# Kernel optimization log

Hardware: AMD Instinct MI355X
Metric: run time of the kernel (lower is better)

## Reference

```python
import jax, jax.numpy as jnp
import numpy as np

H = 1024   # hidden_dim
D = 256    # output_dim
T = 64     # output_len
B = 256    # batch
FC1, FC2 = 1024, 512
EPS = 1e-5


def setup_inputs() -> dict:
    key = jax.random.key(0)
    ks = iter(jax.random.split(key, 32))
    s = 0.05
    p = {}
    p['hidden'] = jax.random.normal(next(ks), (2, B, H), jnp.float32)
    # GRU layer 0: input D -> hidden H ; layer 1: H -> H
    p['W_ih0'] = jax.random.normal(next(ks), (3 * H, D), jnp.float32) * s
    p['W_hh0'] = jax.random.normal(next(ks), (3 * H, H), jnp.float32) * s
    p['b_ih0'] = jax.random.normal(next(ks), (3 * H,), jnp.float32) * s
    p['b_hh0'] = jax.random.normal(next(ks), (3 * H,), jnp.float32) * s
    p['W_ih1'] = jax.random.normal(next(ks), (3 * H, H), jnp.float32) * s
    p['W_hh1'] = jax.random.normal(next(ks), (3 * H, H), jnp.float32) * s
    p['b_ih1'] = jax.random.normal(next(ks), (3 * H,), jnp.float32) * s
    p['b_hh1'] = jax.random.normal(next(ks), (3 * H,), jnp.float32) * s
    # FC head: H -> 1024 -> 512 -> D
    p['fc1_w'] = jax.random.normal(next(ks), (FC1, H), jnp.float32) * s
    p['fc1_b'] = jnp.zeros((FC1,), jnp.float32)
    p['ln1_g'] = jnp.ones((FC1,), jnp.float32)
    p['ln1_b'] = jnp.zeros((FC1,), jnp.float32)
    p['fc2_w'] = jax.random.normal(next(ks), (FC2, FC1), jnp.float32) * s
    p['fc2_b'] = jnp.zeros((FC2,), jnp.float32)
    p['ln2_g'] = jnp.ones((FC2,), jnp.float32)
    p['ln2_b'] = jnp.zeros((FC2,), jnp.float32)
    p['fc3_w'] = jax.random.normal(next(ks), (D, FC2), jnp.float32) * s
    p['fc3_b'] = jnp.zeros((D,), jnp.float32)
    return p


def _gru_cell(x, h, W_ih, W_hh, b_ih, b_hh):
    gi = x @ W_ih.T + b_ih            # [B, 3H]
    gh = h @ W_hh.T + b_hh            # [B, 3H]
    i_r, i_z, i_n = jnp.split(gi, 3, axis=-1)
    h_r, h_z, h_n = jnp.split(gh, 3, axis=-1)
    r = jax.nn.sigmoid(i_r + h_r)
    z = jax.nn.sigmoid(i_z + h_z)
    n = jnp.tanh(i_n + r * h_n)
    return (1.0 - z) * n + z * h


def _layernorm(x, g, b):
    mu = jnp.mean(x, axis=-1, keepdims=True)
    var = jnp.mean(jnp.square(x - mu), axis=-1, keepdims=True)
    return (x - mu) * jax.lax.rsqrt(var + EPS) * g + b


def reference(hidden, W_ih0, W_hh0, b_ih0, b_hh0, W_ih1, W_hh1, b_ih1, b_hh1,
              fc1_w, fc1_b, ln1_g, ln1_b, fc2_w, fc2_b, ln2_g, ln2_b, fc3_w, fc3_b):
    batch = hidden.shape[1]

    def fc_head(x):
        x = jax.nn.gelu(_layernorm(x @ fc1_w.T + fc1_b, ln1_g, ln1_b), approximate=False)
        x = jax.nn.gelu(_layernorm(x @ fc2_w.T + fc2_b, ln2_g, ln2_b), approximate=False)
        return x @ fc3_w.T + fc3_b

    def step(carry, _):
        h0, h1, out = carry
        h0 = _gru_cell(out, h0, W_ih0, W_hh0, b_ih0, b_hh0)
        h1 = _gru_cell(h0, h1, W_ih1, W_hh1, b_ih1, b_hh1)
        out = jax.nn.softmax(fc_head(h1), axis=-1)   # fed back as next input
        return (h0, h1, out), out

    init = (hidden[0], hidden[1], jnp.zeros((batch, D), hidden.dtype))
    _, outs = jax.lax.scan(step, init, None, length=T)   # [T, B, D]
    return jnp.transpose(outs, (1, 0, 2))                # [B, T, D]
```

## Files before the change

### kernel.cpp

```cpp
#include <hip/hip_runtime.h>
#include <math.h>

typedef __bf16 bf16_t;
typedef __bf16 bf16x8 __attribute__((ext_vector_type(8)));
typedef float f32x4 __attribute__((ext_vector_type(4)));

#define B_ 256
#define H_ 1024

template<int NW, int EPI>
__global__ __launch_bounds__(NW * 64) void gemm_mfma(
    const bf16_t* __restrict__ A, const bf16_t* __restrict__ W,
    const float* __restrict__ bias, int K,
    float* __restrict__ C, int ldc,
    float* __restrict__ hf,
    bf16_t* __restrict__ d1, int ld1, int off1,
    bf16_t* __restrict__ d2, int ld2, int off2)
{
    constexpr int MT = NW * 16;
    constexpr int R = 4 / NW;
    __shared__ __align__(16) bf16_t ldsA[2][2][MT * 40];
    __shared__ __align__(16) bf16_t ldsB[2][2][64 * 40];

    int bx = blockIdx.x, by = blockIdx.y;
    if (EPI == 1) {
        int d = by * 64 + bx;
        bx = (d & 7) * 8 + ((d >> 3) & 7);
        by = d >> 6;
    }
    const int bm = by * MT, bn = bx * 64;
    const int tid = threadIdx.x;

    const int srow = tid >> 2, schk = tid & 3;
    const bf16_t* gA = A + (size_t)(bm + srow) * K + schk * 8;
    const bf16_t* gW = W + (size_t)(bn + srow) * K + schk * 8;
    const unsigned sa = srow * 40 + schk * 8;

    const int lane = tid & 63, wv = tid >> 6;
    const int quad = lane >> 4, col = lane & 15;
    const unsigned ra_off = (wv * 16 + col) * 40 + quad * 8;
    const unsigned rb_off = col * 40 + quad * 8;

    f32x4 acc[4];
#pragma unroll
    for (int j = 0; j < 4; j++)
#pragma unroll
        for (int e = 0; e < 4; e++) acc[j][e] = 0.f;

    int4 pa0, pa1, pb0[R], pb1[R];

    pa0 = *(const int4*)gA;
    pa1 = *(const int4*)(gA + 32);
#pragma unroll
    for (int r = 0; r < R; r++) {
        pb0[r] = *(const int4*)(gW + (size_t)(r * MT) * K);
        pb1[r] = *(const int4*)(gW + (size_t)(r * MT) * K + 32);
    }
    gA += 64; gW += 64;

    *(int4*)&ldsA[0][0][sa] = pa0;
    *(int4*)&ldsA[0][1][sa] = pa1;
#pragma unroll
    for (int r = 0; r < R; r++) {
        *(int4*)&ldsB[0][0][sa + r * MT * 40] = pb0[r];
        *(int4*)&ldsB[0][1][sa + r * MT * 40] = pb1[r];
    }

    pa0 = *(const int4*)gA;
    pa1 = *(const int4*)(gA + 32);
#pragma unroll
    for (int r = 0; r < R; r++) {
        pb0[r] = *(const int4*)(gW + (size_t)(r * MT) * K);
        pb1[r] = *(const int4*)(gW + (size_t)(r * MT) * K + 32);
    }
    gA += 64; gW += 64;

    const int nit = K >> 6;
    __syncthreads();

    for (int c = 0; c < nit; ++c) {
        const int cur = c & 1;
        bf16x8 af0 = *(const bf16x8*)&ldsA[cur][0][ra_off];
        bf16x8 af1 = *(const bf16x8*)&ldsA[cur][1][ra_off];
        bf16x8 b00 = *(const bf16x8*)&ldsB[cur][0][rb_off];
        bf16x8 b01 = *(const bf16x8*)&ldsB[cur][0][rb_off + 16 * 40];
        bf16x8 b02 = *(const bf16x8*)&ldsB[cur][0][rb_off + 32 * 40];
        bf16x8 b03 = *(const bf16x8*)&ldsB[cur][0][rb_off + 48 * 40];
        bf16x8 b10 = *(const bf16x8*)&ldsB[cur][1][rb_off];
        bf16x8 b11 = *(const bf16x8*)&ldsB[cur][1][rb_off + 16 * 40];
        bf16x8 b12 = *(const bf16x8*)&ldsB[cur][1][rb_off + 32 * 40];
        bf16x8 b13 = *(const bf16x8*)&ldsB[cur][1][rb_off + 48 * 40];

        if (c + 1 < nit) {
            const int nxt = cur ^ 1;
            *(int4*)&ldsA[nxt][0][sa] = pa0;
            *(int4*)&ldsA[nxt][1][sa] = pa1;
#pragma unroll
            for (int r = 0; r < R; r++) {
                *(int4*)&ldsB[nxt][0][sa + r * MT * 40] = pb0[r];
                *(int4*)&ldsB[nxt][1][sa + r * MT * 40] = pb1[r];
            }
            if (c + 2 < nit) {
                pa0 = *(const int4*)gA;
                pa1 = *(const int4*)(gA + 32);
#pragma unroll
                for (int r = 0; r < R; r++) {
                    pb0[r] = *(const int4*)(gW + (size_t)(r * MT) * K);
                    pb1[r] = *(const int4*)(gW + (size_t)(r * MT) * K + 32);
                }
                gA += 64; gW += 64;
            }
        }

        acc[0] = __builtin_amdgcn_mfma_f32_16x16x32_bf16(af0, b00, acc[0], 0, 0, 0);
        acc[1] = __builtin_amdgcn_mfma_f32_16x16x32_bf16(af0, b01, acc[1], 0, 0, 0);
        acc[2] = __builtin_amdgcn_mfma_f32_16x16x32_bf16(af0, b02, acc[2], 0, 0, 0);
        acc[3] = __builtin_amdgcn_mfma_f32_16x16x32_bf16(af0, b03, acc[3], 0, 0, 0);
        acc[0] = __builtin_amdgcn_mfma_f32_16x16x32_bf16(af1, b10, acc[0], 0, 0, 0);
        acc[1] = __builtin_amdgcn_mfma_f32_16x16x32_bf16(af1, b11, acc[1], 0, 0, 0);
        acc[2] = __builtin_amdgcn_mfma_f32_16x16x32_bf16(af1, b12, acc[2], 0, 0, 0);
        acc[3] = __builtin_amdgcn_mfma_f32_16x16x32_bf16(af1, b13, acc[3], 0, 0, 0);

        __syncthreads();
    }

    if (EPI == 0) {
#pragma unroll
        for (int j = 0; j < 4; j++) {
            const int n = bn + j * 16 + col;
            const float bj = bias[n];
#pragma unroll
            for (int r = 0; r < 4; r++) {
                const int m = bm + wv * 16 + quad * 4 + r;
                C[(size_t)m * ldc + n] = acc[j][r] + bj;
            }
        }
    } else {
        const int cch = (bn >> 2) + col;
        const float br  = bias[bn + col];
        const float bz  = bias[bn + 16 + col];
        const float bin = bias[bn + 32 + col];
        const float bhn = bias[bn + 48 + col];
#pragma unroll
        for (int r = 0; r < 4; r++) {
            const int m = bm + wv * 16 + quad * 4 + r;
            const float gr  = acc[0][r] + br;
            const float gz  = acc[1][r] + bz;
            const float gin = acc[2][r] + bin;
            const float ghn = acc[3][r] + bhn;
            const float rr = 1.f / (1.f + __expf(-gr));
            const float zz = 1.f / (1.f + __expf(-gz));
            const float nn = tanhf(gin + rr * ghn);
            const size_t hidx = (size_t)m * 1024 + cch;
            const float hnew = (1.f - zz) * nn + zz * hf[hidx];
            hf[hidx] = hnew;
            const bf16_t hb = (bf16_t)hnew;
            d1[(size_t)m * ld1 + off1 + cch] = hb;
            d2[(size_t)m * ld2 + off2 + cch] = hb;
        }
    }
}

__global__ __launch_bounds__(256) void build_w4(
    const float* __restrict__ Wih, const float* __restrict__ Whh,
    const float* __restrict__ bih, const float* __restrict__ bhh,
    bf16_t* __restrict__ W4, float* __restrict__ b4, int Kx)
{
    const int K = Kx + 1024;
    const int tpr = K >> 2;
    const int idx = blockIdx.x * 256 + threadIdx.x;
    const int np = idx / tpr;
    const int k4 = (idx - np * tpr) * 4;
    const int c = ((np >> 6) << 4) + (np & 15);
    const int g = (np >> 4) & 3;
    const int srow = (g == 0 ? c : (g == 1 ? 1024 + c : 2048 + c));
    float4 v = make_float4(0.f, 0.f, 0.f, 0.f);
    if (k4 < Kx) {
        if (g != 3) v = *(const float4*)(Wih + (size_t)srow * Kx + k4);
    } else {
        if (g != 2) v = *(const float4*)(Whh + (size_t)srow * 1024 + (k4 - Kx));
    }
    bf16_t* dst = W4 + (size_t)np * K + k4;
    dst[0] = (bf16_t)v.x; dst[1] = (bf16_t)v.y;
    dst[2] = (bf16_t)v.z; dst[3] = (bf16_t)v.w;
    if (k4 == 0) {
        b4[np] = (g == 0) ? bih[c] + bhh[c]
               : (g == 1) ? bih[1024 + c] + bhh[1024 + c]
               : (g == 2) ? bih[2048 + c] : bhh[2048 + c];
    }
}

__global__ __launch_bounds__(256) void conv_bf16(
    const float* __restrict__ src, bf16_t* __restrict__ dst)
{
    const int i4 = (blockIdx.x * 256 + threadIdx.x) * 4;
    float4 v = *(const float4*)(src + i4);
    dst[i4 + 0] = (bf16_t)v.x; dst[i4 + 1] = (bf16_t)v.y;
    dst[i4 + 2] = (bf16_t)v.z; dst[i4 + 3] = (bf16_t)v.w;
}

__global__ __launch_bounds__(256) void init_state(
    const float* __restrict__ hidden, float* __restrict__ h0f,
    float* __restrict__ h1f, bf16_t* __restrict__ A0_0, bf16_t* __restrict__ A1_0)
{
    const int i = blockIdx.x * 256 + threadIdx.x;
    const int m = i >> 10, c = i & 1023;
    const float h0 = hidden[i], h1 = hidden[262144 + i];
    h0f[i] = h0; h1f[i] = h1;
    A0_0[(size_t)m * 1280 + 256 + c] = (bf16_t)h0;
    A1_0[(size_t)m * 2048 + 1024 + c] = (bf16_t)h1;
    if (c < 256) A0_0[(size_t)m * 1280 + c] = (bf16_t)0.f;
}

__device__ __forceinline__ float block_reduce_sum(float v, float* red)
{
#pragma unroll
    for (int o = 32; o > 0; o >>= 1) v += __shfl_xor(v, o, 64);
    const int wid = threadIdx.x >> 6;
    if ((threadIdx.x & 63) == 0) red[wid] = v;
    __syncthreads();
    float s = red[0] + red[1] + red[2] + red[3];
    __syncthreads();
    return s;
}

template <int N>
__global__ __launch_bounds__(256) void ln_gelu(
    const float* __restrict__ X, const float* __restrict__ g,
    const float* __restrict__ b, bf16_t* __restrict__ Y)
{
    __shared__ float red[4];
    const int row = blockIdx.x;
    const int tid = threadIdx.x;
    constexpr int PT = N / 256;
    float v[PT];
    float s = 0.f;
#pragma unroll
    for (int i = 0; i < PT; i++) {
        v[i] = X[(size_t)row * N + tid + i * 256];
        s += v[i];
    }
    const float mu = block_reduce_sum(s, red) * (1.f / N);
    float s2 = 0.f;
#pragma unroll
    for (int i = 0; i < PT; i++) { float d = v[i] - mu; s2 += d * d; }
    const float var = block_reduce_sum(s2, red) * (1.f / N);
    const float inv = rsqrtf(var + 1e-5f);
#pragma unroll
    for (int i = 0; i < PT; i++) {
        const int c = tid + i * 256;
        const float t = (v[i] - mu) * inv * g[c] + b[c];
        Y[(size_t)row * N + c] = (bf16_t)(0.5f * t * (1.f + erff(t * 0.70710678118654752f)));
    }
}

__global__ __launch_bounds__(256) void softmax_fb(
    const float* __restrict__ logits, float* __restrict__ dout,
    bf16_t* __restrict__ a0w, int t)
{
    const int wv = threadIdx.x >> 6, lane = threadIdx.x & 63;
    const int row = blockIdx.x * 4 + wv;
    float v[4];
#pragma unroll
    for (int j = 0; j < 4; j++) v[j] = logits[(size_t)row * 256 + lane + 64 * j];
    float mx = fmaxf(fmaxf(v[0], v[1]), fmaxf(v[2], v[3]));
#pragma unroll
    for (int o = 32; o > 0; o >>= 1) mx = fmaxf(mx, __shfl_xor(mx, o, 64));
    float e[4], s = 0.f;
#pragma unroll
    for (int j = 0; j < 4; j++) { e[j] = expf(v[j] - mx); s += e[j]; }
#pragma unroll
    for (int o = 32; o > 0; o >>= 1) s += __shfl_xor(s, o, 64);
    const float inv = 1.f / s;
#pragma unroll
    for (int j = 0; j < 4; j++) {
        const float p = e[j] * inv;
        const int c = lane + 64 * j;
        dout[((size_t)row * 64 + t) * 256 + c] = p;
        a0w[(size_t)row * 1280 + c] = (bf16_t)p;
    }
}

extern "C" void kernel_launch(void* const* d_in, const int* in_sizes, int n_in,
                              void* d_out, int out_size, void* d_ws, size_t ws_size,
                              hipStream_t stream)
{
    const float* hidden = (const float*)d_in[0];
    const float* W_ih0  = (const float*)d_in[1];
    const float* W_hh0  = (const float*)d_in[2];
    const float* b_ih0  = (const float*)d_in[3];
    const float* b_hh0  = (const float*)d_in[4];
    const float* W_ih1  = (const float*)d_in[5];
    const float* W_hh1  = (const float*)d_in[6];
    const float* b_ih1  = (const float*)d_in[7];
    const float* b_hh1  = (const float*)d_in[8];
    const float* fc1_w  = (const float*)d_in[9];
    const float* fc1_b  = (const float*)d_in[10];
    const float* ln1_g  = (const float*)d_in[11];
    const float* ln1_b  = (const float*)d_in[12];
    const float* fc2_w  = (const float*)d_in[13];
    const float* fc2_b  = (const float*)d_in[14];
    const float* ln2_g  = (const float*)d_in[15];
    const float* ln2_b  = (const float*)d_in[16];
    const float* fc3_w  = (const float*)d_in[17];
    const float* fc3_b  = (const float*)d_in[18];
    float* dout = (float*)d_out;

    char* p = (char*)d_ws;
    auto alloc = [&](size_t bytes) { void* r = (void*)p; p += (bytes + 255) & ~(size_t)255; return r; };
    float*  h0f   = (float*)alloc(262144 * 4);
    float*  h1f   = (float*)alloc(262144 * 4);
    bf16_t* A0[2] = { (bf16_t*)alloc(256 * 1280 * 2), (bf16_t*)alloc(256 * 1280 * 2) };
    bf16_t* A1[2] = { (bf16_t*)alloc(256 * 2048 * 2), (bf16_t*)alloc(256 * 2048 * 2) };
    bf16_t* h1b   = (bf16_t*)alloc(262144 * 2);
    float*  a1r   = (float*)alloc(262144 * 4);
    bf16_t* a1b   = (bf16_t*)alloc(262144 * 2);
    float*  a2r   = (float*)alloc(131072 * 4);
    bf16_t* a2b   = (bf16_t*)alloc(131072 * 2);
    float*  logits= (float*)alloc(65536 * 4);
    float*  b4_0  = (float*)alloc(4096 * 4);
    float*  b4_1  = (float*)alloc(4096 * 4);
    bf16_t* W4_0  = (bf16_t*)alloc((size_t)4096 * 1280 * 2);
    bf16_t* W4_1  = (bf16_t*)alloc((size_t)4096 * 2048 * 2);
    bf16_t* fc1wb = (bf16_t*)alloc((size_t)1048576 * 2);
    bf16_t* fc2wb = (bf16_t*)alloc((size_t)524288 * 2);
    bf16_t* fc3wb = (bf16_t*)alloc((size_t)131072 * 2);

    build_w4<<<5120, 256, 0, stream>>>(W_ih0, W_hh0, b_ih0, b_hh0, W4_0, b4_0, 256);
    build_w4<<<8192, 256, 0, stream>>>(W_ih1, W_hh1, b_ih1, b_hh1, W4_1, b4_1, 1024);
    conv_bf16<<<1024, 256, 0, stream>>>(fc1_w, fc1wb);
    conv_bf16<<<512, 256, 0, stream>>>(fc2_w, fc2wb);
    conv_bf16<<<128, 256, 0, stream>>>(fc3_w, fc3wb);
    init_state<<<1024, 256, 0, stream>>>(hidden, h0f, h1f, A0[0], A1[0]);

    for (int t = 0; t < 64; t++) {
        bf16_t* A0r = A0[t & 1];
        bf16_t* A0w = A0[(t + 1) & 1];
        bf16_t* A1r = A1[t & 1];
        bf16_t* A1w = A1[(t + 1) & 1];

        gemm_mfma<4, 1><<<dim3(64, 4), 256, 0, stream>>>(
            A0r, W4_0, b4_0, 1280, nullptr, 0,
            h0f, A1r, 2048, 0, A0w, 1280, 256);
        gemm_mfma<4, 1><<<dim3(64, 4), 256, 0, stream>>>(
            A1r, W4_1, b4_1, 2048, nullptr, 0,
            h1f, A1w, 2048, 1024, h1b, 1024, 0);
        gemm_mfma<2, 0><<<dim3(16, 8), 128, 0, stream>>>(
            h1b, fc1wb, fc1_b, 1024, a1r, 1024, nullptr, nullptr, 0, 0, nullptr, 0, 0);
        ln_gelu<1024><<<256, 256, 0, stream>>>(a1r, ln1_g, ln1_b, a1b);
        gemm_mfma<2, 0><<<dim3(8, 8), 128, 0, stream>>>(
            a1b, fc2wb, fc2_b, 1024, a2r, 512, nullptr, nullptr, 0, 0, nullptr, 0, 0);
        ln_gelu<512><<<256, 256, 0, stream>>>(a2r, ln2_g, ln2_b, a2b);
        gemm_mfma<2, 0><<<dim3(4, 8), 128, 0, stream>>>(
            a2b, fc3wb, fc3_b, 512, logits, 256, nullptr, nullptr, 0, 0, nullptr, 0, 0);
        softmax_fb<<<64, 256, 0, stream>>>(logits, dout, A0w, t);
    }
}
```

Measured before the change: 4.652 ms.

## Fuse second LayerNorm-GELU, fc3 GEMM and softmax into one kernel

Replaces the per-step ln_gelu<512>, fc3 GEMM and softmax kernels with a single fused kernel. Each 16-row block normalizes and applies GELU into LDS, runs an MFMA GEMM over the full fc3 weight, then does the softmax and writes both the output and the bf16 feedback. This removes two launches per step and the intermediate global buffers. In exchange it uses only 16 blocks, each streaming the entire fc3 weight, which may limit parallelism.

Measured after the change: 5.511 ms. 1.18x slower.

```diff
diff --git a/kernel.cpp b/kernel.cpp
--- a/kernel.cpp
+++ b/kernel.cpp
@@ -161,6 +161,169 @@
     }
 }
 
+__global__ __launch_bounds__(256) void fc3_head(
+    const float* __restrict__ X,
+    const float* __restrict__ g, const float* __restrict__ b,
+    const bf16_t* __restrict__ W,
+    const float* __restrict__ bias,
+    float* __restrict__ dout, bf16_t* __restrict__ a0w, int t)
+{
+    __shared__ __align__(16) bf16_t ldsA[16 * 520];
+    __shared__ __align__(16) bf16_t ldsB[2][2][256 * 40];
+    __shared__ float lgt[16][264];
+
+    const int tid = threadIdx.x;
+    const int rb = blockIdx.x * 16;
+
+    {
+        const int row = tid >> 4, l16 = tid & 15;
+        const float* xr = X + (size_t)(rb + row) * 512;
+        float4 v[8];
+        float s = 0.f;
+#pragma unroll
+        for (int i = 0; i < 8; i++) {
+            v[i] = *(const float4*)(xr + l16 * 4 + i * 64);
+            s += v[i].x + v[i].y + v[i].z + v[i].w;
+        }
+#pragma unroll
+        for (int o = 1; o < 16; o <<= 1) s += __shfl_xor(s, o, 64);
+        const float mu = s * (1.f / 512.f);
+        float s2 = 0.f;
+#pragma unroll
+        for (int i = 0; i < 8; i++) {
+            float dx = v[i].x - mu, dy = v[i].y - mu;
+            float dz = v[i].z - mu, dw = v[i].w - mu;
+            s2 += dx * dx + dy * dy + dz * dz + dw * dw;
+        }
+#pragma unroll
+        for (int o = 1; o < 16; o <<= 1) s2 += __shfl_xor(s2, o, 64);
+        const float inv = rsqrtf(s2 * (1.f / 512.f) + 1e-5f);
+#pragma unroll
+        for (int i = 0; i < 8; i++) {
+            const int c = l16 * 4 + i * 64;
+            float e[4] = { v[i].x, v[i].y, v[i].z, v[i].w };
+            bf16_t* dst = ldsA + row * 520 + c;
+#pragma unroll
+            for (int q = 0; q < 4; q++) {
+                const float tq = (e[q] - mu) * inv * g[c + q] + b[c + q];
+                dst[q] = (bf16_t)(0.5f * tq * (1.f + erff(tq * 0.70710678118654752f)));
+            }
+        }
+    }
+
+    const int lane = tid & 63, wv = tid >> 6;
+    const int quad = lane >> 4, col16 = lane & 15;
+    const unsigned ra_base = col16 * 520 + quad * 8;
+    const unsigned rb_base = (wv * 64 + col16) * 40 + quad * 8;
+
+    const int r0 = tid >> 2, chk = tid & 3;
+    const bf16_t* gW0 = W + (size_t)r0 * 512 + chk * 8;
+    const unsigned sb = r0 * 40 + chk * 8;
+
+    f32x4 acc[4];
+#pragma unroll
+    for (int j = 0; j < 4; j++)
+#pragma unroll
+        for (int e = 0; e < 4; e++) acc[j][e] = 0.f;
+
+    int4 pb[2][4];
+#pragma unroll
+    for (int h = 0; h < 2; h++)
+#pragma unroll
+        for (int p = 0; p < 4; p++)
+            pb[h][p] = *(const int4*)(gW0 + (size_t)(p * 64) * 512 + h * 32);
+#pragma unroll
+    for (int h = 0; h < 2; h++)
+#pragma unroll
+        for (int p = 0; p < 4; p++)
+            *(int4*)&ldsB[0][h][sb + p * 64 * 40] = pb[h][p];
+#pragma unroll
+    for (int h = 0; h < 2; h++)
+#pragma unroll
+        for (int p = 0; p < 4; p++)
+            pb[h][p] = *(const int4*)(gW0 + (size_t)(p * 64) * 512 + 64 + h * 32);
+
+    __syncthreads();
+
+    for (int it = 0; it < 8; ++it) {
+        const int cur = it & 1;
+        bf16x8 af0 = *(const bf16x8*)(ldsA + ra_base + it * 64);
+        bf16x8 af1 = *(const bf16x8*)(ldsA + ra_base + it * 64 + 32);
+        bf16x8 b00 = *(const bf16x8*)&ldsB[cur][0][rb_base];
+        bf16x8 b01 = *(const bf16x8*)&ldsB[cur][0][rb_base + 16 * 40];
+        bf16x8 b02 = *(const bf16x8*)&ldsB[cur][0][rb_base + 32 * 40];
+        bf16x8 b03 = *(const bf16x8*)&ldsB[cur][0][rb_base + 48 * 40];
+        bf16x8 b10 = *(const bf16x8*)&ldsB[cur][1][rb_base];
+        bf16x8 b11 = *(const bf16x8*)&ldsB[cur][1][rb_base + 16 * 40];
+        bf16x8 b12 = *(const bf16x8*)&ldsB[cur][1][rb_base + 32 * 40];
+        bf16x8 b13 = *(const bf16x8*)&ldsB[cur][1][rb_base + 48 * 40];
+
+        if (it + 1 < 8) {
+            const int nxt = cur ^ 1;
+#pragma unroll
+            for (int h = 0; h < 2; h++)
+#pragma unroll
+                for (int p = 0; p < 4; p++)
+                    *(int4*)&ldsB[nxt][h][sb + p * 64 * 40] = pb[h][p];
+            if (it + 2 < 8) {
+#pragma unroll
+                for (int h = 0; h < 2; h++)
+#pragma unroll
+                    for (int p = 0; p < 4; p++)
+                        pb[h][p] = *(const int4*)(gW0 + (size_t)(p * 64) * 512 + (it + 2) * 64 + h * 32);
+            }
+        }
+
+        acc[0] = __builtin_amdgcn_mfma_f32_16x16x32_bf16(af0, b00, acc[0], 0, 0, 0);
+        acc[1] = __builtin_amdgcn_mfma_f32_16x16x32_bf16(af0, b01, acc[1], 0, 0, 0);
+        acc[2] = __builtin_amdgcn_mfma_f32_16x16x32_bf16(af0, b02, acc[2], 0, 0, 0);
+        acc[3] = __builtin_amdgcn_mfma_f32_16x16x32_bf16(af0, b03, acc[3], 0, 0, 0);
+        acc[0] = __builtin_amdgcn_mfma_f32_16x16x32_bf16(af1, b10, acc[0], 0, 0, 0);
+        acc[1] = __builtin_amdgcn_mfma_f32_16x16x32_bf16(af1, b11, acc[1], 0, 0, 0);
+        acc[2] = __builtin_amdgcn_mfma_f32_16x16x32_bf16(af1, b12, acc[2], 0, 0, 0);
+        acc[3] = __builtin_amdgcn_mfma_f32_16x16x32_bf16(af1, b13, acc[3], 0, 0, 0);
+
+        __syncthreads();
+    }
+
+#pragma unroll
+    for (int j = 0; j < 4; j++) {
+        const int n = wv * 64 + j * 16 + col16;
+        const float bj = bias[n];
+#pragma unroll
+        for (int r = 0; r < 4; r++)
+            lgt[quad * 4 + r][n] = acc[j][r] + bj;
+    }
+    __syncthreads();
+
+    {
+        const int row = tid >> 4, l16 = tid & 15;
+        float vv[16];
+        float mx = -1e30f;
+#pragma unroll
+        for (int j = 0; j < 16; j++) {
+            vv[j] = lgt[row][l16 + j * 16];
+            mx = fmaxf(mx, vv[j]);
+        }
+#pragma unroll
+        for (int o = 1; o < 16; o <<= 1) mx = fmaxf(mx, __shfl_xor(mx, o, 64));
+        float ss = 0.f;
+#pragma unroll
+        for (int j = 0; j < 16; j++) { vv[j] = expf(vv[j] - mx); ss += vv[j]; }
+#pragma unroll
+        for (int o = 1; o < 16; o <<= 1) ss += __shfl_xor(ss, o, 64);
+        const float isv = 1.f / ss;
+        const int m = rb + row;
+#pragma unroll
+        for (int j = 0; j < 16; j++) {
+            const float pv = vv[j] * isv;
+            const int c = l16 + j * 16;
+            dout[((size_t)m * 64 + t) * 256 + c] = pv;
+            a0w[(size_t)m * 1280 + c] = (bf16_t)pv;
+        }
+    }
+}
+
 __global__ __launch_bounds__(256) void build_w4(
     const float* __restrict__ Wih, const float* __restrict__ Whh,
     const float* __restrict__ bih, const float* __restrict__ bhh,
@@ -251,33 +414,6 @@
         const int c = tid + i * 256;
         const float t = (v[i] - mu) * inv * g[c] + b[c];
         Y[(size_t)row * N + c] = (bf16_t)(0.5f * t * (1.f + erff(t * 0.70710678118654752f)));
-    }
-}
-
-__global__ __launch_bounds__(256) void softmax_fb(
-    const float* __restrict__ logits, float* __restrict__ dout,
-    bf16_t* __restrict__ a0w, int t)
-{
-    const int wv = threadIdx.x >> 6, lane = threadIdx.x & 63;
-    const int row = blockIdx.x * 4 + wv;
-    float v[4];
-#pragma unroll
-    for (int j = 0; j < 4; j++) v[j] = logits[(size_t)row * 256 + lane + 64 * j];
-    float mx = fmaxf(fmaxf(v[0], v[1]), fmaxf(v[2], v[3]));
-#pragma unroll
-    for (int o = 32; o > 0; o >>= 1) mx = fmaxf(mx, __shfl_xor(mx, o, 64));
-    float e[4], s = 0.f;
-#pragma unroll
-    for (int j = 0; j < 4; j++) { e[j] = expf(v[j] - mx); s += e[j]; }
-#pragma unroll
-    for (int o = 32; o > 0; o >>= 1) s += __shfl_xor(s, o, 64);
-    const float inv = 1.f / s;
-#pragma unroll
-    for (int j = 0; j < 4; j++) {
-        const float p = e[j] * inv;
-        const int c = lane + 64 * j;
-        dout[((size_t)row * 64 + t) * 256 + c] = p;
-        a0w[(size_t)row * 1280 + c] = (bf16_t)p;
     }
 }
 
@@ -316,8 +452,6 @@
     float*  a1r   = (float*)alloc(262144 * 4);
     bf16_t* a1b   = (bf16_t*)alloc(262144 * 2);
     float*  a2r   = (float*)alloc(131072 * 4);
-    bf16_t* a2b   = (bf16_t*)alloc(131072 * 2);
-    float*  logits= (float*)alloc(65536 * 4);
     float*  b4_0  = (float*)alloc(4096 * 4);
     float*  b4_1  = (float*)alloc(4096 * 4);
     bf16_t* W4_0  = (bf16_t*)alloc((size_t)4096 * 1280 * 2);
@@ -350,9 +484,6 @@
         ln_gelu<1024><<<256, 256, 0, stream>>>(a1r, ln1_g, ln1_b, a1b);
         gemm_mfma<2, 0><<<dim3(8, 8), 128, 0, stream>>>(
             a1b, fc2wb, fc2_b, 1024, a2r, 512, nullptr, nullptr, 0, 0, nullptr, 0, 0);
-        ln_gelu<512><<<256, 256, 0, stream>>>(a2r, ln2_g, ln2_b, a2b);
-        gemm_mfma<2, 0><<<dim3(4, 8), 128, 0, stream>>>(
-            a2b, fc3wb, fc3_b, 512, logits, 256, nullptr, nullptr, 0, 0, nullptr, 0, 0);
-        softmax_fb<<<64, 256, 0, stream>>>(logits, dout, A0w, t);
-    }
-}
+        fc3_head<<<16, 256, 0, stream>>>(a2r, ln2_g, ln2_b, fc3wb, fc3_b, dout, A0w, t);
+    }
+}
```

## Split GRU GEMM tiles across 8 waves with shuffle-based gate epilogue

Applied to the files above, without the earlier changes.

Adds a dedicated GRU GEMM kernel with 512 threads per block, where 8 waves each compute a 16x32 slice of the 64x64 tile instead of 4 waves each computing 16x64. The packed weight layout is reordered so gates interleave in groups of 8 columns, and the epilogue gathers r/z/n gate values across lanes with xor shuffles. The aim is more waves per block to hide latency in the latency-bound recurrent GEMMs. The cost is lower per-wave MFMA work, extra shuffles, and half the lanes idle during the elementwise update.

New measurement: 4.685 ms. Within noise of the previous version (+0.7%).

```diff
diff --git a/kernel.cpp b/kernel.cpp
--- a/kernel.cpp
+++ b/kernel.cpp
@@ -8,27 +8,117 @@
 #define B_ 256
 #define H_ 1024
 
-template<int NW, int EPI>
+__global__ __launch_bounds__(512) void gru_gemm(
+    const bf16_t* __restrict__ A, const bf16_t* __restrict__ W,
+    const float* __restrict__ bias, int K,
+    float* __restrict__ hf,
+    bf16_t* __restrict__ d1, int ld1, int off1,
+    bf16_t* __restrict__ d2, int ld2, int off2)
+{
+    __shared__ __align__(16) bf16_t ldsA[2][2][64 * 40];
+    __shared__ __align__(16) bf16_t ldsB[2][2][64 * 40];
+
+    int bx = blockIdx.x, by = blockIdx.y;
+    {
+        int d = by * 64 + bx;
+        bx = (d & 7) * 8 + ((d >> 3) & 7);
+        by = d >> 6;
+    }
+    const int bm = by * 64, bn = bx * 64;
+    const int tid = threadIdx.x;
+
+    const int srow = tid >> 3, schk = tid & 7;
+    const int shalf = schk >> 2;
+    const unsigned so = srow * 40 + (schk & 3) * 8;
+    const bf16_t* gA = A + (size_t)(bm + srow) * K + schk * 8;
+    const bf16_t* gW = W + (size_t)(bn + srow) * K + schk * 8;
+
+    const int lane = tid & 63, wv = tid >> 6;
+    const int rg = wv >> 1, chh = wv & 1;
+    const int quad = lane >> 4, col = lane & 15;
+    const unsigned ra = (rg * 16 + col) * 40 + quad * 8;
+    const unsigned rb = (chh * 32 + col) * 40 + quad * 8;
+
+    f32x4 acc0, acc1;
+#pragma unroll
+    for (int e = 0; e < 4; e++) { acc0[e] = 0.f; acc1[e] = 0.f; }
+
+    int4 pa, pb;
+    pa = *(const int4*)gA; pb = *(const int4*)gW; gA += 64; gW += 64;
+    *(int4*)&ldsA[0][shalf][so] = pa;
+    *(int4*)&ldsB[0][shalf][so] = pb;
+    pa = *(const int4*)gA; pb = *(const int4*)gW; gA += 64; gW += 64;
+
+    const int nit = K >> 6;
+    __syncthreads();
+
+    for (int c = 0; c < nit; ++c) {
+        const int cur = c & 1;
+        bf16x8 af0 = *(const bf16x8*)&ldsA[cur][0][ra];
+        bf16x8 af1 = *(const bf16x8*)&ldsA[cur][1][ra];
+        bf16x8 b00 = *(const bf16x8*)&ldsB[cur][0][rb];
+        bf16x8 b01 = *(const bf16x8*)&ldsB[cur][0][rb + 16 * 40];
+        bf16x8 b10 = *(const bf16x8*)&ldsB[cur][1][rb];
+        bf16x8 b11 = *(const bf16x8*)&ldsB[cur][1][rb + 16 * 40];
+
+        if (c + 1 < nit) {
+            const int nxt = cur ^ 1;
+            *(int4*)&ldsA[nxt][shalf][so] = pa;
+            *(int4*)&ldsB[nxt][shalf][so] = pb;
+            if (c + 2 < nit) {
+                pa = *(const int4*)gA; pb = *(const int4*)gW;
+                gA += 64; gW += 64;
+            }
+        }
+
+        acc0 = __builtin_amdgcn_mfma_f32_16x16x32_bf16(af0, b00, acc0, 0, 0, 0);
+        acc1 = __builtin_amdgcn_mfma_f32_16x16x32_bf16(af0, b01, acc1, 0, 0, 0);
+        acc0 = __builtin_amdgcn_mfma_f32_16x16x32_bf16(af1, b10, acc0, 0, 0, 0);
+        acc1 = __builtin_amdgcn_mfma_f32_16x16x32_bf16(af1, b11, acc1, 0, 0, 0);
+
+        __syncthreads();
+    }
+
+    const int cch = (bn >> 2) + chh * 8 + (col & 7);
+    const float b0 = bias[bn + chh * 32 + col];
+    const float b1 = bias[bn + chh * 32 + 16 + col];
+#pragma unroll
+    for (int r = 0; r < 4; r++) {
+        const int m = bm + rg * 16 + quad * 4 + r;
+        const float a0 = acc0[r] + b0;
+        const float a1 = acc1[r] + b1;
+        const float p0 = __shfl_xor(a0, 8, 64);
+        const float p1 = __shfl_xor(a1, 8, 64);
+        const float gr  = (col < 8) ? a0 : p0;
+        const float gz  = (col < 8) ? p0 : a0;
+        const float gin = (col < 8) ? a1 : p1;
+        const float ghn = (col < 8) ? p1 : a1;
+        const float rr = 1.f / (1.f + __expf(-gr));
+        const float zz = 1.f / (1.f + __expf(-gz));
+        const float nn = tanhf(gin + rr * ghn);
+        if (col < 8) {
+            const size_t hidx = (size_t)m * 1024 + cch;
+            const float hnew = (1.f - zz) * nn + zz * hf[hidx];
+            hf[hidx] = hnew;
+            const bf16_t hb = (bf16_t)hnew;
+            d1[(size_t)m * ld1 + off1 + cch] = hb;
+            d2[(size_t)m * ld2 + off2 + cch] = hb;
+        }
+    }
+}
+
+template<int NW>
 __global__ __launch_bounds__(NW * 64) void gemm_mfma(
     const bf16_t* __restrict__ A, const bf16_t* __restrict__ W,
     const float* __restrict__ bias, int K,
-    float* __restrict__ C, int ldc,
-    float* __restrict__ hf,
-    bf16_t* __restrict__ d1, int ld1, int off1,
-    bf16_t* __restrict__ d2, int ld2, int off2)
+    float* __restrict__ C, int ldc)
 {
     constexpr int MT = NW * 16;
     constexpr int R = 4 / NW;
     __shared__ __align__(16) bf16_t ldsA[2][2][MT * 40];
     __shared__ __align__(16) bf16_t ldsB[2][2][64 * 40];
 
-    int bx = blockIdx.x, by = blockIdx.y;
-    if (EPI == 1) {
-        int d = by * 64 + bx;
-        bx = (d & 7) * 8 + ((d >> 3) & 7);
-        by = d >> 6;
-    }
-    const int bm = by * MT, bn = bx * 64;
+    const int bm = blockIdx.y * MT, bn = blockIdx.x * 64;
     const int tid = threadIdx.x;
 
     const int srow = tid >> 2, schk = tid & 3;
@@ -124,39 +214,14 @@
         __syncthreads();
     }
 
-    if (EPI == 0) {
-#pragma unroll
-        for (int j = 0; j < 4; j++) {
-            const int n = bn + j * 16 + col;
-            const float bj = bias[n];
-#pragma unroll
-            for (int r = 0; r < 4; r++) {
-                const int m = bm + wv * 16 + quad * 4 + r;
-                C[(size_t)m * ldc + n] = acc[j][r] + bj;
-            }
-        }
-    } else {
-        const int cch = (bn >> 2) + col;
-        const float br  = bias[bn + col];
-        const float bz  = bias[bn + 16 + col];
-        const float bin = bias[bn + 32 + col];
-        const float bhn = bias[bn + 48 + col];
+#pragma unroll
+    for (int j = 0; j < 4; j++) {
+        const int n = bn + j * 16 + col;
+        const float bj = bias[n];
 #pragma unroll
         for (int r = 0; r < 4; r++) {
             const int m = bm + wv * 16 + quad * 4 + r;
-            const float gr  = acc[0][r] + br;
-            const float gz  = acc[1][r] + bz;
-            const float gin = acc[2][r] + bin;
-            const float ghn = acc[3][r] + bhn;
-            const float rr = 1.f / (1.f + __expf(-gr));
-            const float zz = 1.f / (1.f + __expf(-gz));
-            const float nn = tanhf(gin + rr * ghn);
-            const size_t hidx = (size_t)m * 1024 + cch;
-            const float hnew = (1.f - zz) * nn + zz * hf[hidx];
-            hf[hidx] = hnew;
-            const bf16_t hb = (bf16_t)hnew;
-            d1[(size_t)m * ld1 + off1 + cch] = hb;
-            d2[(size_t)m * ld2 + off2 + cch] = hb;
+            C[(size_t)m * ldc + n] = acc[j][r] + bj;
         }
     }
 }
@@ -171,8 +236,10 @@
     const int idx = blockIdx.x * 256 + threadIdx.x;
     const int np = idx / tpr;
     const int k4 = (idx - np * tpr) * 4;
-    const int c = ((np >> 6) << 4) + (np & 15);
-    const int g = (np >> 4) & 3;
+    const int lo = np & 7;
+    const int g = (np >> 3) & 3;
+    const int hi = (np >> 5) & 1;
+    const int c = ((np >> 6) << 4) + (hi << 3) + lo;
     const int srow = (g == 0 ? c : (g == 1 ? 1024 + c : 2048 + c));
     float4 v = make_float4(0.f, 0.f, 0.f, 0.f);
     if (k4 < Kx) {
@@ -339,20 +406,20 @@
         bf16_t* A1r = A1[t & 1];
         bf16_t* A1w = A1[(t + 1) & 1];
 
-        gemm_mfma<4, 1><<<dim3(64, 4), 256, 0, stream>>>(
-            A0r, W4_0, b4_0, 1280, nullptr, 0,
+        gru_gemm<<<dim3(64, 4), 512, 0, stream>>>(
+            A0r, W4_0, b4_0, 1280,
             h0f, A1r, 2048, 0, A0w, 1280, 256);
-        gemm_mfma<4, 1><<<dim3(64, 4), 256, 0, stream>>>(
-            A1r, W4_1, b4_1, 2048, nullptr, 0,
+        gru_gemm<<<dim3(64, 4), 512, 0, stream>>>(
+            A1r, W4_1, b4_1, 2048,
             h1f, A1w, 2048, 1024, h1b, 1024, 0);
-        gemm_mfma<2, 0><<<dim3(16, 8), 128, 0, stream>>>(
-            h1b, fc1wb, fc1_b, 1024, a1r, 1024, nullptr, nullptr, 0, 0, nullptr, 0, 0);
+        gemm_mfma<2><<<dim3(16, 8), 128, 0, stream>>>(
+            h1b, fc1wb, fc1_b, 1024, a1r, 1024);
         ln_gelu<1024><<<256, 256, 0, stream>>>(a1r, ln1_g, ln1_b, a1b);
-        gemm_mfma<2, 0><<<dim3(8, 8), 128, 0, stream>>>(
-            a1b, fc2wb, fc2_b, 1024, a2r, 512, nullptr, nullptr, 0, 0, nullptr, 0, 0);
+        gemm_mfma<2><<<dim3(8, 8), 128, 0, stream>>>(
+            a1b, fc2wb, fc2_b, 1024, a2r, 512);
         ln_gelu<512><<<256, 256, 0, stream>>>(a2r, ln2_g, ln2_b, a2b);
-        gemm_mfma<2, 0><<<dim3(4, 8), 128, 0, stream>>>(
-            a2b, fc3wb, fc3_b, 512, logits, 256, nullptr, nullptr, 0, 0, nullptr, 0, 0);
+        gemm_mfma<2><<<dim3(4, 8), 128, 0, stream>>>(
+            a2b, fc3wb, fc3_b, 512, logits, 256);
         softmax_fb<<<64, 256, 0, stream>>>(logits, dout, A0w, t);
     }
 }
```

## Fuse softmax feedback into next step's layer-0 GRU GEMM prologue

Applied to the files above, without the earlier changes.

Drops the per-step softmax kernel. Each layer-0 GRU GEMM block of the next step recomputes the softmax of its 64 rows of logits into shared memory and takes the first 256 K-columns of A from there instead of global memory. Block column 0 also writes the fp32 output for the previous step, and a single softmax launch after the loop handles the final step. This saves one launch and one sync point per step, but every one of the 64 column blocks now repeats the same softmax work, and the prologue adds shared-memory use.

Result: slower. 4.963 ms (+6.7%).

```diff
diff --git a/kernel.cpp b/kernel.cpp
--- a/kernel.cpp
+++ b/kernel.cpp
@@ -5,22 +5,23 @@
 typedef __bf16 bf16x8 __attribute__((ext_vector_type(8)));
 typedef float f32x4 __attribute__((ext_vector_type(4)));
 
-#define B_ 256
-#define H_ 1024
-
-template<int NW, int EPI>
+#define SMP 272
+
+template<int NW, int EPI, int SM>
 __global__ __launch_bounds__(NW * 64) void gemm_mfma(
     const bf16_t* __restrict__ A, const bf16_t* __restrict__ W,
     const float* __restrict__ bias, int K,
     float* __restrict__ C, int ldc,
     float* __restrict__ hf,
     bf16_t* __restrict__ d1, int ld1, int off1,
-    bf16_t* __restrict__ d2, int ld2, int off2)
+    bf16_t* __restrict__ d2, int ld2, int off2,
+    const float* __restrict__ logits, float* __restrict__ dsm, int tprev)
 {
     constexpr int MT = NW * 16;
     constexpr int R = 4 / NW;
     __shared__ __align__(16) bf16_t ldsA[2][2][MT * 40];
     __shared__ __align__(16) bf16_t ldsB[2][2][64 * 40];
+    __shared__ __align__(16) bf16_t smA[SM ? 64 * SMP : 8];
 
     int bx = blockIdx.x, by = blockIdx.y;
     if (EPI == 1) {
@@ -31,9 +32,51 @@
     const int bm = by * MT, bn = bx * 64;
     const int tid = threadIdx.x;
 
+    if constexpr (SM) {
+        const int prow = tid >> 2, part = tid & 3;
+        const float* lg = logits + (size_t)(bm + prow) * 256 + part * 64;
+        float4 v[16];
+        float mx = -1e30f;
+#pragma unroll
+        for (int i = 0; i < 16; i++) {
+            v[i] = *(const float4*)(lg + i * 4);
+            mx = fmaxf(mx, fmaxf(fmaxf(v[i].x, v[i].y), fmaxf(v[i].z, v[i].w)));
+        }
+        mx = fmaxf(mx, __shfl_xor(mx, 1, 64));
+        mx = fmaxf(mx, __shfl_xor(mx, 2, 64));
+        float s = 0.f;
+#pragma unroll
+        for (int i = 0; i < 16; i++) {
+            v[i].x = expf(v[i].x - mx); v[i].y = expf(v[i].y - mx);
+            v[i].z = expf(v[i].z - mx); v[i].w = expf(v[i].w - mx);
+            s += v[i].x + v[i].y + v[i].z + v[i].w;
+        }
+        s += __shfl_xor(s, 1, 64);
+        s += __shfl_xor(s, 2, 64);
+        const float inv = 1.f / s;
+        bf16_t* dsts = smA + prow * SMP + part * 64;
+#pragma unroll
+        for (int i = 0; i < 16; i++) {
+            dsts[i * 4 + 0] = (bf16_t)(v[i].x * inv);
+            dsts[i * 4 + 1] = (bf16_t)(v[i].y * inv);
+            dsts[i * 4 + 2] = (bf16_t)(v[i].z * inv);
+            dsts[i * 4 + 3] = (bf16_t)(v[i].w * inv);
+        }
+        if (bx == 0) {
+            float* o = dsm + ((size_t)(bm + prow) * 64 + tprev) * 256 + part * 64;
+#pragma unroll
+            for (int i = 0; i < 16; i++) {
+                float4 pv = make_float4(v[i].x * inv, v[i].y * inv,
+                                        v[i].z * inv, v[i].w * inv);
+                *(float4*)(o + i * 4) = pv;
+            }
+        }
+        __syncthreads();
+    }
+
     const int srow = tid >> 2, schk = tid & 3;
-    const bf16_t* gA = A + (size_t)(bm + srow) * K + schk * 8;
-    const bf16_t* gW = W + (size_t)(bn + srow) * K + schk * 8;
+    const bf16_t* gA0 = A + (size_t)(bm + srow) * K + schk * 8;
+    const bf16_t* gW0 = W + (size_t)(bn + srow) * K + schk * 8;
     const unsigned sa = srow * 40 + schk * 8;
 
     const int lane = tid & 63, wv = tid >> 6;
@@ -47,16 +90,30 @@
 #pragma unroll
         for (int e = 0; e < 4; e++) acc[j][e] = 0.f;
 
+    auto loadA = [&](int cc, int4& qa0, int4& qa1) {
+        if (SM && cc < 4) {
+            const bf16_t* sp = smA + srow * SMP + cc * 64 + schk * 8;
+            qa0 = *(const int4*)sp;
+            qa1 = *(const int4*)(sp + 32);
+        } else {
+            const bf16_t* g = gA0 + (size_t)cc * 64;
+            qa0 = *(const int4*)g;
+            qa1 = *(const int4*)(g + 32);
+        }
+    };
+    auto loadW = [&](int cc, int4* qb0, int4* qb1) {
+#pragma unroll
+        for (int r = 0; r < R; r++) {
+            const bf16_t* g = gW0 + (size_t)(r * MT) * K + (size_t)cc * 64;
+            qb0[r] = *(const int4*)g;
+            qb1[r] = *(const int4*)(g + 32);
+        }
+    };
+
     int4 pa0, pa1, pb0[R], pb1[R];
 
-    pa0 = *(const int4*)gA;
-    pa1 = *(const int4*)(gA + 32);
-#pragma unroll
-    for (int r = 0; r < R; r++) {
-        pb0[r] = *(const int4*)(gW + (size_t)(r * MT) * K);
-        pb1[r] = *(const int4*)(gW + (size_t)(r * MT) * K + 32);
-    }
-    gA += 64; gW += 64;
+    loadA(0, pa0, pa1);
+    loadW(0, pb0, pb1);
 
     *(int4*)&ldsA[0][0][sa] = pa0;
     *(int4*)&ldsA[0][1][sa] = pa1;
@@ -66,14 +123,8 @@
         *(int4*)&ldsB[0][1][sa + r * MT * 40] = pb1[r];
     }
 
-    pa0 = *(const int4*)gA;
-    pa1 = *(const int4*)(gA + 32);
-#pragma unroll
-    for (int r = 0; r < R; r++) {
-        pb0[r] = *(const int4*)(gW + (size_t)(r * MT) * K);
-        pb1[r] = *(const int4*)(gW + (size_t)(r * MT) * K + 32);
-    }
-    gA += 64; gW += 64;
+    loadA(1, pa0, pa1);
+    loadW(1, pb0, pb1);
 
     const int nit = K >> 6;
     __syncthreads();
@@ -101,14 +152,8 @@
                 *(int4*)&ldsB[nxt][1][sa + r * MT * 40] = pb1[r];
             }
             if (c + 2 < nit) {
-                pa0 = *(const int4*)gA;
-                pa1 = *(const int4*)(gA + 32);
-#pragma unroll
-                for (int r = 0; r < R; r++) {
-                    pb0[r] = *(const int4*)(gW + (size_t)(r * MT) * K);
-                    pb1[r] = *(const int4*)(gW + (size_t)(r * MT) * K + 32);
-                }
-                gA += 64; gW += 64;
+                loadA(c + 2, pa0, pa1);
+                loadW(c + 2, pb0, pb1);
             }
         }
 
@@ -339,20 +384,29 @@
         bf16_t* A1r = A1[t & 1];
         bf16_t* A1w = A1[(t + 1) & 1];
 
-        gemm_mfma<4, 1><<<dim3(64, 4), 256, 0, stream>>>(
-            A0r, W4_0, b4_0, 1280, nullptr, 0,
-            h0f, A1r, 2048, 0, A0w, 1280, 256);
-        gemm_mfma<4, 1><<<dim3(64, 4), 256, 0, stream>>>(
+        if (t == 0) {
+            gemm_mfma<4, 1, 0><<<dim3(64, 4), 256, 0, stream>>>(
+                A0r, W4_0, b4_0, 1280, nullptr, 0,
+                h0f, A1r, 2048, 0, A0w, 1280, 256, nullptr, nullptr, 0);
+        } else {
+            gemm_mfma<4, 1, 1><<<dim3(64, 4), 256, 0, stream>>>(
+                A0r, W4_0, b4_0, 1280, nullptr, 0,
+                h0f, A1r, 2048, 0, A0w, 1280, 256, logits, dout, t - 1);
+        }
+        gemm_mfma<4, 1, 0><<<dim3(64, 4), 256, 0, stream>>>(
             A1r, W4_1, b4_1, 2048, nullptr, 0,
-            h1f, A1w, 2048, 1024, h1b, 1024, 0);
-        gemm_mfma<2, 0><<<dim3(16, 8), 128, 0, stream>>>(
-            h1b, fc1wb, fc1_b, 1024, a1r, 1024, nullptr, nullptr, 0, 0, nullptr, 0, 0);
+            h1f, A1w, 2048, 1024, h1b, 1024, 0, nullptr, nullptr, 0);
+        gemm_mfma<2, 0, 0><<<dim3(16, 8), 128, 0, stream>>>(
+            h1b, fc1wb, fc1_b, 1024, a1r, 1024,
+            nullptr, nullptr, 0, 0, nullptr, 0, 0, nullptr, nullptr, 0);
         ln_gelu<1024><<<256, 256, 0, stream>>>(a1r, ln1_g, ln1_b, a1b);
-        gemm_mfma<2, 0><<<dim3(8, 8), 128, 0, stream>>>(
-            a1b, fc2wb, fc2_b, 1024, a2r, 512, nullptr, nullptr, 0, 0, nullptr, 0, 0);
+        gemm_mfma<2, 0, 0><<<dim3(8, 8), 128, 0, stream>>>(
+            a1b, fc2wb, fc2_b, 1024, a2r, 512,
+            nullptr, nullptr, 0, 0, nullptr, 0, 0, nullptr, nullptr, 0);
         ln_gelu<512><<<256, 256, 0, stream>>>(a2r, ln2_g, ln2_b, a2b);
-        gemm_mfma<2, 0><<<dim3(4, 8), 128, 0, stream>>>(
-            a2b, fc3wb, fc3_b, 512, logits, 256, nullptr, nullptr, 0, 0, nullptr, 0, 0);
-        softmax_fb<<<64, 256, 0, stream>>>(logits, dout, A0w, t);
-    }
-}
+        gemm_mfma<2, 0, 0><<<dim3(4, 8), 128, 0, stream>>>(
+            a2b, fc3wb, fc3_b, 512, logits, 256,
+            nullptr, nullptr, 0, 0, nullptr, 0, 0, nullptr, nullptr, 0);
+    }
+    softmax_fb<<<64, 256, 0, stream>>>(logits, dout, A0[0], 63);
+}
```
